# Performance work log

Measured on AMD Instinct MI355X. Metric: run time of the kernel, lower is better.

## Reference

```python
import jax, jax.numpy as jnp
import numpy as np

VOCAB, VDIM, DDIM, BATCH = 50257, 300, 512, 16


def setup_inputs() -> dict:
    key = jax.random.key(0)
    k1, k2, k3, k4, k5 = jax.random.split(key, 5)
    return {
        "decoder_hidden": jax.random.normal(k1, (BATCH, DDIM), dtype=jnp.float32),
        "embedding_vocab": jax.random.normal(k2, (VOCAB, VDIM), dtype=jnp.float32),
        "W_dec": jax.random.normal(k3, (VDIM, DDIM), dtype=jnp.float32) * (1.0 / np.sqrt(DDIM)),
        "b_dec": jax.random.normal(k4, (VDIM,), dtype=jnp.float32) * 0.01,
        "W_full": jax.random.normal(k5, (VDIM,), dtype=jnp.float32) * (1.0 / np.sqrt(VDIM)),
        "b_full": jnp.zeros((), dtype=jnp.float32),
    }


def reference(decoder_hidden, embedding_vocab, W_dec, b_dec, W_full, b_full):
    # query: (B, vocab_dim) = decoder_att(decoder_hidden)
    query = decoder_hidden @ W_dec.T + b_dec
    # additive scores: relu(vocab + query) projected to scalar -> (B, V)
    hidden = jax.nn.relu(embedding_vocab[None, :, :] + query[:, None, :])  # (B, V, D)
    att = jnp.einsum("bvd,d->bv", hidden, W_full) + b_full
    alpha = jax.nn.softmax(att, axis=1)  # softmax over vocab
    # weighted sum of vocab embeddings: (B, vocab_dim)
    attention_weighted_encoding = jnp.einsum("bv,vd->bd", alpha, embedding_vocab)
    return attention_weighted_encoding, alpha
```

## Files before the change

### kernel.cpp

```cpp
#include <hip/hip_runtime.h>

constexpr int V  = 50257;
constexpr int D  = 300;
constexpr int KD = 512;
constexpr int B  = 16;

constexpr int ROWS = 32;
constexpr int NB_ATT = (V + ROWS - 1) / ROWS;
constexpr int NC  = 512;
constexpr int RPC = (V + NC - 1) / NC;

constexpr float NEG_HUGE = -1.0e30f;

constexpr size_t WS_QT   = 0;
constexpr size_t WS_STAT = 4800;
constexpr size_t WS_MS   = WS_STAT + (size_t)NB_ATT * 32;
constexpr size_t WS_PART = WS_MS + 32;
constexpr size_t WS_TMP  = WS_PART + (size_t)NC * 4800;

struct f4 { float v[4]; };
__device__ __forceinline__ f4 ld4(const float* p) {
    float4 t = *(const float4*)p;
    return {t.x, t.y, t.z, t.w};
}

__global__ void __launch_bounds__(256) k_query(
    const float* __restrict__ dh, const float* __restrict__ Wdec,
    const float* __restrict__ bdec, float* __restrict__ q_t)
{
    int wid  = (blockIdx.x * 256 + threadIdx.x) >> 6;
    int lane = threadIdx.x & 63;
    if (wid >= D * B) return;
    int d = wid >> 4, b = wid & 15;
    const float* wrow = Wdec + (size_t)d * KD;
    const float* hrow = dh + (size_t)b * KD;
    float s = 0.f;
    for (int k = lane; k < KD; k += 64) s += wrow[k] * hrow[k];
    #pragma unroll
    for (int off = 32; off; off >>= 1) s += __shfl_down(s, off, 64);
    if (lane == 0) q_t[d * 16 + b] = s + bdec[d];
}

__global__ void __launch_bounds__(256, 6) k_att(
    const float* __restrict__ E, const float* __restrict__ q_t,
    const float* __restrict__ wf, const float* __restrict__ bf,
    float* __restrict__ att, float* __restrict__ blkstats)
{
    __shared__ float sq[4800];
    __shared__ float sw[304];
    int t = threadIdx.x;
    for (int i4 = t * 4; i4 < 4800; i4 += 1024) {
        float4 qv = *(const float4*)(q_t + i4);
        int d = i4 >> 4, bq = (i4 & 15) >> 2;
        int col = (bq + (d >> 2)) & 3;
        *(float4*)(sq + (d << 4) + (col << 2)) = qv;
    }
    for (int i = t; i < 304; i += 256) sw[i] = (i < 300) ? wf[i] : 0.f;
    __syncthreads();

    const int bg   = t >> 6;
    const int lane = t & 63;
    const int rs   = lane >> 2;
    const int p    = lane & 3;
    const int p4   = p << 2;
    const int rot4 = ((bg + p) & 3) << 2;
    const int v0   = blockIdx.x << 5;

    const float* ep[2];
    bool rvalid[2];
    #pragma unroll
    for (int j = 0; j < 2; ++j) {
        int row = v0 + rs + (j << 4);
        rvalid[j] = row < V;
        ep[j] = E + (size_t)(rvalid[j] ? row : (V - 1)) * D;
    }

    float acc[2][4];
    #pragma unroll
    for (int j = 0; j < 2; ++j)
        #pragma unroll
        for (int b = 0; b < 4; ++b) acc[j][b] = 0.f;

    f4 ec[2], en[2];
    #pragma unroll
    for (int j = 0; j < 2; ++j) ec[j] = ld4(ep[j] + p4);

    for (int k = 0; k < 19; ++k) {
        int d0 = (k << 4) + p4;
        bool cur_ok = d0 < D;
        int dn = d0 + 16;
        int dns = (dn < D) ? dn : p4;
        #pragma unroll
        for (int j = 0; j < 2; ++j) en[j] = ld4(ep[j] + dns);
        if (cur_ok) {
            f4 wv = ld4(sw + d0);
            #pragma unroll
            for (int i = 0; i < 4; ++i) {
                f4 qv = ld4(sq + ((d0 + i) << 4) + rot4);
                float wi = wv.v[i];
                #pragma unroll
                for (int j = 0; j < 2; ++j) {
                    float e = ec[j].v[i];
                    #pragma unroll
                    for (int b = 0; b < 4; ++b)
                        acc[j][b] = fmaf(fmaxf(e + qv.v[b], 0.f), wi, acc[j][b]);
                }
            }
        }
        #pragma unroll
        for (int j = 0; j < 2; ++j) ec[j] = en[j];
    }

    #pragma unroll
    for (int j = 0; j < 2; ++j)
        #pragma unroll
        for (int b = 0; b < 4; ++b) {
            float s = acc[j][b];
            s += __shfl_xor(s, 1, 64);
            s += __shfl_xor(s, 2, 64);
            acc[j][b] = s;
        }

    float bfull = bf[0];
    float vj[2];
    float m_l = NEG_HUGE;
    #pragma unroll
    for (int j = 0; j < 2; ++j) {
        float s = (p == 0) ? acc[j][0] : (p == 1) ? acc[j][1]
                : (p == 2) ? acc[j][2] : acc[j][3];
        s += bfull;
        int row = v0 + rs + (j << 4);
        if (rvalid[j]) att[(size_t)((bg << 2) + p) * V + row] = s;
        vj[j] = rvalid[j] ? s : NEG_HUGE;
        m_l = fmaxf(m_l, vj[j]);
    }
    float s_l = __expf(vj[0] - m_l) + __expf(vj[1] - m_l);

    #pragma unroll
    for (int sh = 2; sh < 6; ++sh) {
        int mask = 1 << sh;
        float mo = __shfl_xor(m_l, mask, 64);
        float so = __shfl_xor(s_l, mask, 64);
        float mn = fmaxf(m_l, mo);
        s_l = s_l * __expf(m_l - mn) + so * __expf(mo - mn);
        m_l = mn;
    }
    if (rs == 0) {
        size_t idx = ((size_t)blockIdx.x * 16 + (bg << 2) + p) * 2;
        blkstats[idx]     = m_l;
        blkstats[idx + 1] = s_l;
    }
}

__global__ void __launch_bounds__(64) k_combine(
    const float* __restrict__ blkstats, float* __restrict__ MS)
{
    int b = blockIdx.x, lane = threadIdx.x;
    float m = NEG_HUGE;
    for (int c = lane; c < NB_ATT; c += 64)
        m = fmaxf(m, blkstats[(size_t)(c * 16 + b) * 2]);
    #pragma unroll
    for (int off = 32; off; off >>= 1) m = fmaxf(m, __shfl_xor(m, off, 64));
    float s = 0.f;
    for (int c = lane; c < NB_ATT; c += 64)
        s += blkstats[(size_t)(c * 16 + b) * 2 + 1] *
             __expf(blkstats[(size_t)(c * 16 + b) * 2] - m);
    #pragma unroll
    for (int off = 32; off; off >>= 1) s += __shfl_xor(s, off, 64);
    if (lane == 0) { MS[b * 2] = m; MS[b * 2 + 1] = 1.f / s; }
}

__global__ void __launch_bounds__(256) k_alpha(
    float* __restrict__ att, const float* __restrict__ MS)
{
    int b = blockIdx.y;
    int v = blockIdx.x * 256 + threadIdx.x;
    if (v >= V) return;
    float M = MS[b * 2], invS = MS[b * 2 + 1];
    size_t i = (size_t)b * V + v;
    att[i] = __expf(att[i] - M) * invS;
}

__global__ void __launch_bounds__(320) k_wsum(
    const float* __restrict__ E, const float* __restrict__ alpha,
    float* __restrict__ partials)
{
    int c = blockIdx.x, t = threadIdx.x;
    if (t >= D) return;
    int v0 = c * RPC, v1 = min(v0 + RPC, V);
    float acc[16];
    #pragma unroll
    for (int b = 0; b < 16; ++b) acc[b] = 0.f;
    int v = v0;
    for (; v + 8 <= v1; v += 8) {
        float e[8];
        #pragma unroll
        for (int r = 0; r < 8; ++r) e[r] = E[(size_t)(v + r) * D + t];
        #pragma unroll
        for (int b = 0; b < 16; ++b) {
            const float* ap = alpha + (size_t)b * V + v;
            float a = acc[b];
            #pragma unroll
            for (int r = 0; r < 8; ++r) a = fmaf(ap[r], e[r], a);
            acc[b] = a;
        }
    }
    for (; v < v1; ++v) {
        float e = E[(size_t)v * D + t];
        #pragma unroll
        for (int b = 0; b < 16; ++b)
            acc[b] = fmaf(alpha[(size_t)b * V + v], e, acc[b]);
    }
    #pragma unroll
    for (int b = 0; b < 16; ++b)
        partials[(size_t)c * 4800 + b * D + t] = acc[b];
}

__global__ void __launch_bounds__(256) k_red1(
    const float* __restrict__ partials, float* __restrict__ tmp)
{
    int o4 = blockIdx.x * 256 + threadIdx.x;
    if (o4 >= 1200) return;
    int y = blockIdx.y;
    float4 s = {0.f, 0.f, 0.f, 0.f};
    for (int c = y * 32; c < y * 32 + 32; ++c) {
        float4 p = *(const float4*)(partials + (size_t)c * 4800 + o4 * 4);
        s.x += p.x; s.y += p.y; s.z += p.z; s.w += p.w;
    }
    *(float4*)(tmp + (size_t)y * 4800 + o4 * 4) = s;
}

__global__ void __launch_bounds__(256) k_red2(
    const float* __restrict__ tmp, float* __restrict__ out)
{
    int o4 = blockIdx.x * 256 + threadIdx.x;
    if (o4 >= 1200) return;
    float4 s = {0.f, 0.f, 0.f, 0.f};
    #pragma unroll
    for (int y = 0; y < 16; ++y) {
        float4 p = *(const float4*)(tmp + (size_t)y * 4800 + o4 * 4);
        s.x += p.x; s.y += p.y; s.z += p.z; s.w += p.w;
    }
    *(float4*)(out + o4 * 4) = s;
}

extern "C" void kernel_launch(void* const* d_in, const int* in_sizes, int n_in,
                              void* d_out, int out_size, void* d_ws, size_t ws_size,
                              hipStream_t stream) {
    const float* dh   = (const float*)d_in[0];
    const float* E    = (const float*)d_in[1];
    const float* Wdec = (const float*)d_in[2];
    const float* bdec = (const float*)d_in[3];
    const float* wf   = (const float*)d_in[4];
    const float* bf   = (const float*)d_in[5];
    float* out = (float*)d_out;
    float* ws  = (float*)d_ws;

    float* q_t   = ws + WS_QT;
    float* stats = ws + WS_STAT;
    float* MS    = ws + WS_MS;
    float* part  = ws + WS_PART;
    float* tmp   = ws + WS_TMP;
    float* att   = out + 4800;

    k_query<<<(D * B + 3) / 4, 256, 0, stream>>>(dh, Wdec, bdec, q_t);
    k_att<<<NB_ATT, 256, 0, stream>>>(E, q_t, wf, bf, att, stats);
    k_combine<<<B, 64, 0, stream>>>(stats, MS);
    k_alpha<<<dim3((V + 255) / 256, B), 256, 0, stream>>>(att, MS);
    k_wsum<<<NC, 320, 0, stream>>>(E, att, part);
    k_red1<<<dim3(5, 16), 256, 0, stream>>>(part, tmp);
    k_red2<<<5, 256, 0, stream>>>(tmp, out);
}
```

Before: 84.81 us.

## Fuse softmax normalization into weighted-sum kernel and drop att loop bound checks

Merges the separate alpha normalization kernel into the weighted-sum kernel. Each block now computes its slice of alpha, writes it back, and stages it in shared memory as a transposed v-by-b tile, so the inner loop reads vectorized alpha from LDS instead of strided global loads. The attention kernel pads the shared query buffer with zeros so the per-iteration bound branch can be removed, unrolls its loop by two and drops the occupancy hint in launch bounds. This removes one launch and one global pass over alpha, at the cost of a block-wide sync, extra shared memory, and possibly higher register use in the attention kernel.

```diff
diff --git a/kernel.cpp b/kernel.cpp
--- a/kernel.cpp
+++ b/kernel.cpp
@@ -41,12 +41,12 @@
     if (lane == 0) q_t[d * 16 + b] = s + bdec[d];
 }
 
-__global__ void __launch_bounds__(256, 6) k_att(
+__global__ void __launch_bounds__(256) k_att(
     const float* __restrict__ E, const float* __restrict__ q_t,
     const float* __restrict__ wf, const float* __restrict__ bf,
     float* __restrict__ att, float* __restrict__ blkstats)
 {
-    __shared__ float sq[4800];
+    __shared__ float sq[4864];
     __shared__ float sw[304];
     int t = threadIdx.x;
     for (int i4 = t * 4; i4 < 4800; i4 += 1024) {
@@ -55,6 +55,7 @@
         int col = (bq + (d >> 2)) & 3;
         *(float4*)(sq + (d << 4) + (col << 2)) = qv;
     }
+    if (t < 64) sq[4800 + t] = 0.f;
     for (int i = t; i < 304; i += 256) sw[i] = (i < 300) ? wf[i] : 0.f;
     __syncthreads();
 
@@ -85,26 +86,25 @@
     #pragma unroll
     for (int j = 0; j < 2; ++j) ec[j] = ld4(ep[j] + p4);
 
+    #pragma unroll 2
     for (int k = 0; k < 19; ++k) {
         int d0 = (k << 4) + p4;
-        bool cur_ok = d0 < D;
         int dn = d0 + 16;
-        int dns = (dn < D) ? dn : p4;
+        int dns = (dn < D) ? dn : 0;
         #pragma unroll
         for (int j = 0; j < 2; ++j) en[j] = ld4(ep[j] + dns);
-        if (cur_ok) {
-            f4 wv = ld4(sw + d0);
+
+        f4 wv = ld4(sw + d0);
+        #pragma unroll
+        for (int i = 0; i < 4; ++i) {
+            f4 qv = ld4(sq + ((d0 + i) << 4) + rot4);
+            float wi = wv.v[i];
             #pragma unroll
-            for (int i = 0; i < 4; ++i) {
-                f4 qv = ld4(sq + ((d0 + i) << 4) + rot4);
-                float wi = wv.v[i];
+            for (int j = 0; j < 2; ++j) {
+                float e = ec[j].v[i];
                 #pragma unroll
-                for (int j = 0; j < 2; ++j) {
-                    float e = ec[j].v[i];
-                    #pragma unroll
-                    for (int b = 0; b < 4; ++b)
-                        acc[j][b] = fmaf(fmaxf(e + qv.v[b], 0.f), wi, acc[j][b]);
-                }
+                for (int b = 0; b < 4; ++b)
+                    acc[j][b] = fmaf(fmaxf(e + qv.v[b], 0.f), wi, acc[j][b]);
             }
         }
         #pragma unroll
@@ -170,50 +170,51 @@
     if (lane == 0) { MS[b * 2] = m; MS[b * 2 + 1] = 1.f / s; }
 }
 
-__global__ void __launch_bounds__(256) k_alpha(
-    float* __restrict__ att, const float* __restrict__ MS)
-{
-    int b = blockIdx.y;
-    int v = blockIdx.x * 256 + threadIdx.x;
-    if (v >= V) return;
-    float M = MS[b * 2], invS = MS[b * 2 + 1];
-    size_t i = (size_t)b * V + v;
-    att[i] = __expf(att[i] - M) * invS;
-}
-
-__global__ void __launch_bounds__(320) k_wsum(
-    const float* __restrict__ E, const float* __restrict__ alpha,
-    float* __restrict__ partials)
-{
+__global__ void __launch_bounds__(320) k_awsum(
+    const float* __restrict__ E, float* __restrict__ att,
+    const float* __restrict__ MS, float* __restrict__ partials)
+{
+    __shared__ float sal[RPC * 16];
     int c = blockIdx.x, t = threadIdx.x;
-    if (t >= D) return;
-    int v0 = c * RPC, v1 = min(v0 + RPC, V);
-    float acc[16];
-    #pragma unroll
-    for (int b = 0; b < 16; ++b) acc[b] = 0.f;
-    int v = v0;
-    for (; v + 8 <= v1; v += 8) {
-        float e[8];
-        #pragma unroll
-        for (int r = 0; r < 8; ++r) e[r] = E[(size_t)(v + r) * D + t];
-        #pragma unroll
-        for (int b = 0; b < 16; ++b) {
-            const float* ap = alpha + (size_t)b * V + v;
-            float a = acc[b];
+    int v0 = c * RPC;
+    int n = V - v0;
+    if (n > RPC) n = RPC;
+    if (n < 0) n = 0;
+
+    for (int i = t; i < RPC * 16; i += 320) {
+        int b = i / RPC, vv = i - b * RPC;
+        float a = 0.f;
+        if (vv < n) {
+            float M = MS[b * 2], invS = MS[b * 2 + 1];
+            size_t gi = (size_t)b * V + v0 + vv;
+            a = __expf(att[gi] - M) * invS;
+            att[gi] = a;
+        }
+        sal[vv * 16 + b] = a;
+    }
+    __syncthreads();
+
+    if (t < D) {
+        float acc[16];
+        #pragma unroll
+        for (int b = 0; b < 16; ++b) acc[b] = 0.f;
+        #pragma unroll 4
+        for (int vv = 0; vv < n; ++vv) {
+            float e = E[(size_t)(v0 + vv) * D + t];
+            const float* ap = sal + vv * 16;
+            f4 a0 = ld4(ap), a1 = ld4(ap + 4), a2 = ld4(ap + 8), a3 = ld4(ap + 12);
             #pragma unroll
-            for (int r = 0; r < 8; ++r) a = fmaf(ap[r], e[r], a);
-            acc[b] = a;
-        }
-    }
-    for (; v < v1; ++v) {
-        float e = E[(size_t)v * D + t];
+            for (int b = 0; b < 4; ++b) {
+                acc[b]      = fmaf(a0.v[b], e, acc[b]);
+                acc[b + 4]  = fmaf(a1.v[b], e, acc[b + 4]);
+                acc[b + 8]  = fmaf(a2.v[b], e, acc[b + 8]);
+                acc[b + 12] = fmaf(a3.v[b], e, acc[b + 12]);
+            }
+        }
         #pragma unroll
         for (int b = 0; b < 16; ++b)
-            acc[b] = fmaf(alpha[(size_t)b * V + v], e, acc[b]);
-    }
-    #pragma unroll
-    for (int b = 0; b < 16; ++b)
-        partials[(size_t)c * 4800 + b * D + t] = acc[b];
+            partials[(size_t)c * 4800 + b * D + t] = acc[b];
+    }
 }
 
 __global__ void __launch_bounds__(256) k_red1(
@@ -266,8 +267,7 @@
     k_query<<<(D * B + 3) / 4, 256, 0, stream>>>(dh, Wdec, bdec, q_t);
     k_att<<<NB_ATT, 256, 0, stream>>>(E, q_t, wf, bf, att, stats);
     k_combine<<<B, 64, 0, stream>>>(stats, MS);
-    k_alpha<<<dim3((V + 255) / 256, B), 256, 0, stream>>>(att, MS);
-    k_wsum<<<NC, 320, 0, stream>>>(E, att, part);
+    k_awsum<<<NC, 320, 0, stream>>>(E, att, MS, part);
     k_red1<<<dim3(5, 16), 256, 0, stream>>>(part, tmp);
     k_red2<<<5, 256, 0, stream>>>(tmp, out);
 }
```

Result: faster. 73.43 us (-13.4%).
